# Optimization experiments

Hardware: AMD Instinct MI355X
Metric: run time of the kernel (lower is better)

Reference implementation:

```python
import jax, jax.numpy as jnp
import numpy as np

FILTERS = 256
B, H, W = 16, 64, 64
LN_EPS = 1e-5


def setup_inputs() -> dict:
    key = jax.random.key(0)
    ks = jax.random.split(key, 6)
    C = FILTERS
    scale = 1.0 / np.sqrt(C)  # kaiming-ish init for 1x1 convs
    return {
        "x": jax.random.normal(ks[0], (B, C, H, W), dtype=jnp.float32),
        "g": jax.random.normal(ks[1], (B, C, H, W), dtype=jnp.float32),
        "Wx": jax.random.normal(ks[2], (C, C), dtype=jnp.float32) * scale,
        "Wg": jax.random.normal(ks[3], (C, C), dtype=jnp.float32) * scale,
        "Wpsi": jax.random.normal(ks[4], (1, C), dtype=jnp.float32) * scale,
        "ln_gamma": jnp.ones((C,), dtype=jnp.float32),
        "ln_beta": jnp.zeros((C,), dtype=jnp.float32),
        "bxg": jnp.zeros((C,), dtype=jnp.float32),
        "bpsi": jnp.zeros((1,), dtype=jnp.float32),
    }


def reference(x, g, Wx, Wg, Wpsi, ln_gamma, ln_beta, bxg, bpsi):
    # 1x1 convs == per-pixel channel GEMMs: [B,C,H,W] x [O,C] -> [B,O,H,W]
    x_conv = jnp.einsum("bchw,oc->bohw", x, Wx)
    g_conv = jnp.einsum("bchw,oc->bohw", g, Wg)
    att = jax.nn.relu(x_conv + g_conv + bxg[None, :, None, None])
    # LayerNorm over channel dim (original permutes to NHWC, LN over last dim)
    mean = jnp.mean(att, axis=1, keepdims=True)
    var = jnp.mean(jnp.square(att - mean), axis=1, keepdims=True)
    att = (att - mean) * jax.lax.rsqrt(var + LN_EPS)
    att = att * ln_gamma[None, :, None, None] + ln_beta[None, :, None, None]
    # psi: 1x1 conv to single channel + bias, sigmoid gate
    att = jnp.einsum("bchw,oc->bohw", att, Wpsi) + bpsi[None, :, None, None]
    att = jax.nn.sigmoid(att)  # [B,1,H,W]
    return att * x
```

## Files before the change

kernel.cpp:

```cpp
#include <hip/hip_runtime.h>
#include <stdint.h>


typedef __bf16 bf16x8 __attribute__((ext_vector_type(8)));
typedef float f32x4 __attribute__((ext_vector_type(4)));

#define STR2 264
#define LN_EPS 1e-5f

__device__ __forceinline__ uint16_t f2b(float f) {
    union { float f; uint32_t i; } v; v.f = f;
    uint32_t x = v.i;
    return (uint16_t)((x + 0x7FFFu + ((x >> 16) & 1u)) >> 16);
}

struct EpiShared {
    float red[3][4][64];
    float cpart[8];
};

union ALds {
    uint16_t a[2][64 * STR2];
    EpiShared e;
};

__global__ void wconv_kernel(const float* __restrict__ Wx, const float* __restrict__ Wg,
                             uint16_t* __restrict__ ox, uint16_t* __restrict__ og) {
    const int i  = blockIdx.x * 256 + threadIdx.x;
    const int n  = i >> 6;
    const int k4 = (i & 63) * 4;
    const int it = k4 >> 5;
    const int kk = k4 & 31;
    const int dst = it * 8192 + n * 32 + kk;
    const float4 a = *(const float4*)&Wx[n * 256 + k4];
    const float4 b = *(const float4*)&Wg[n * 256 + k4];
    uint2 pa, pb;
    pa.x = (uint32_t)f2b(a.x) | ((uint32_t)f2b(a.y) << 16);
    pa.y = (uint32_t)f2b(a.z) | ((uint32_t)f2b(a.w) << 16);
    pb.x = (uint32_t)f2b(b.x) | ((uint32_t)f2b(b.y) << 16);
    pb.y = (uint32_t)f2b(b.z) | ((uint32_t)f2b(b.w) << 16);
    *(uint2*)&ox[dst] = pa;
    *(uint2*)&og[dst] = pb;
}

__global__ __launch_bounds__(512, 4) void attgate_psi(
    const float* __restrict__ x,
    const float* __restrict__ g,
    const uint16_t* __restrict__ Wxb,
    const uint16_t* __restrict__ Wgb,
    const float* __restrict__ Wpsi,
    const float* __restrict__ gamma,
    const float* __restrict__ beta,
    const float* __restrict__ bxg,
    const float* __restrict__ bpsi,
    float* __restrict__ psi_g)
{
    __shared__ __align__(16) ALds u;

    const int t    = threadIdx.x;
    const int lane = t & 63;
    const int wv   = t >> 6;
    const int os   = wv & 3;
    const int ps   = wv >> 2;
    const int ln   = lane & 15;
    const int q    = lane >> 4;

    const int gp0  = blockIdx.x * 64;
    const int b    = gp0 >> 12;
    const int pix0 = gp0 & 4095;
    const size_t xbase = (size_t)b * (256 * 4096) + pix0;

    const int at  = t & 255;
    const int px  = at & 63;
    const int cg  = at >> 6;
    const int c0  = cg * 8;
    const float* Asrc = (t < 256) ? x : g;
    const int tens    = (t < 256) ? 0 : 1;

    float av[64];
    #pragma unroll
    for (int it = 0; it < 8; ++it)
        #pragma unroll
        for (int c = 0; c < 8; ++c)
            av[it * 8 + c] = Asrc[xbase + (size_t)(it * 32 + c0 + c) * 4096 + px];

    uint16_t* dstrow = &u.a[tens][px * STR2];
    #pragma unroll
    for (int it = 0; it < 8; ++it) {
        uint4 w;
        w.x = (uint32_t)f2b(av[it*8+0]) | ((uint32_t)f2b(av[it*8+1]) << 16);
        w.y = (uint32_t)f2b(av[it*8+2]) | ((uint32_t)f2b(av[it*8+3]) << 16);
        w.z = (uint32_t)f2b(av[it*8+4]) | ((uint32_t)f2b(av[it*8+5]) << 16);
        w.w = (uint32_t)f2b(av[it*8+6]) | ((uint32_t)f2b(av[it*8+7]) << 16);
        *(uint4*)&dstrow[it * 32 + c0] = w;
    }

    f32x4 acc[2][4];
    #pragma unroll
    for (int i = 0; i < 2; ++i)
        #pragma unroll
        for (int j = 0; j < 4; ++j)
            acc[i][j] = (f32x4){0.f, 0.f, 0.f, 0.f};

    const int fro = os * 64 + ln;

    __syncthreads();

    #pragma unroll
    for (int it = 0; it < 8; ++it) {
        const uint16_t* Wxi = Wxb + it * 8192;
        const uint16_t* Wgi = Wgb + it * 8192;

        bf16x8 bx[4];
        #pragma unroll
        for (int nt = 0; nt < 4; ++nt)
            bx[nt] = *(const bf16x8*)&Wxi[(fro + nt * 16) * 32 + q * 8];

        bf16x8 af[2];
        #pragma unroll
        for (int mt = 0; mt < 2; ++mt)
            af[mt] = *(const bf16x8*)&u.a[0][(ps * 32 + mt * 16 + ln) * STR2 + it * 32 + q * 8];
        #pragma unroll
        for (int mt = 0; mt < 2; ++mt)
            #pragma unroll
            for (int nt = 0; nt < 4; ++nt)
                acc[mt][nt] = __builtin_amdgcn_mfma_f32_16x16x32_bf16(af[mt], bx[nt], acc[mt][nt], 0, 0, 0);

        bf16x8 bg[4];
        #pragma unroll
        for (int nt = 0; nt < 4; ++nt)
            bg[nt] = *(const bf16x8*)&Wgi[(fro + nt * 16) * 32 + q * 8];
        #pragma unroll
        for (int mt = 0; mt < 2; ++mt)
            af[mt] = *(const bf16x8*)&u.a[1][(ps * 32 + mt * 16 + ln) * STR2 + it * 32 + q * 8];
        #pragma unroll
        for (int mt = 0; mt < 2; ++mt)
            #pragma unroll
            for (int nt = 0; nt < 4; ++nt)
                acc[mt][nt] = __builtin_amdgcn_mfma_f32_16x16x32_bf16(af[mt], bg[nt], acc[mt][nt], 0, 0, 0);
    }

    __syncthreads();

    if (t < 256) {
        float a  = Wpsi[t] * gamma[t];
        float bb = Wpsi[t] * beta[t];
        #pragma unroll
        for (int off = 32; off; off >>= 1) {
            a  += __shfl_xor(a, off, 64);
            bb += __shfl_xor(bb, off, 64);
        }
        if (lane == 0) { u.e.cpart[wv] = a; u.e.cpart[4 + wv] = bb; }
    }

    float biasv[4], Ac[4];
    #pragma unroll
    for (int nt = 0; nt < 4; ++nt) {
        const int o = os * 64 + nt * 16 + ln;
        biasv[nt] = bxg[o];
        Ac[nt]    = Wpsi[o] * gamma[o];
    }
    __syncthreads();
    const float sumA = u.e.cpart[0] + u.e.cpart[1] + u.e.cpart[2] + u.e.cpart[3];
    const float sumB = u.e.cpart[4] + u.e.cpart[5] + u.e.cpart[6] + u.e.cpart[7];

    #pragma unroll
    for (int mt = 0; mt < 2; ++mt) {
        #pragma unroll
        for (int r = 0; r < 4; ++r) {
            float s = 0.f, ss = 0.f, tt = 0.f;
            #pragma unroll
            for (int nt = 0; nt < 4; ++nt) {
                float v = acc[mt][nt][r] + biasv[nt];
                v = fmaxf(v, 0.f);
                s += v; ss += v * v; tt += Ac[nt] * v;
            }
            #pragma unroll
            for (int off = 1; off < 16; off <<= 1) {
                s  += __shfl_xor(s,  off, 64);
                ss += __shfl_xor(ss, off, 64);
                tt += __shfl_xor(tt, off, 64);
            }
            if (ln == 0) {
                const int pix = ps * 32 + mt * 16 + q * 4 + r;
                u.e.red[0][os][pix] = s;
                u.e.red[1][os][pix] = ss;
                u.e.red[2][os][pix] = tt;
            }
        }
    }
    __syncthreads();

    if (t < 64) {
        const float s  = u.e.red[0][0][t] + u.e.red[0][1][t] + u.e.red[0][2][t] + u.e.red[0][3][t];
        const float ss = u.e.red[1][0][t] + u.e.red[1][1][t] + u.e.red[1][2][t] + u.e.red[1][3][t];
        const float tt = u.e.red[2][0][t] + u.e.red[2][1][t] + u.e.red[2][2][t] + u.e.red[2][3][t];
        const float mu   = s * (1.f / 256.f);
        const float var  = ss * (1.f / 256.f) - mu * mu;
        const float rstd = rsqrtf(var + LN_EPS);
        const float z    = rstd * (tt - mu * sumA) + sumB + bpsi[0];
        psi_g[gp0 + t] = 1.f / (1.f + __expf(-z));
    }
}

__global__ __launch_bounds__(256) void gate_mul(
    const float* __restrict__ x,
    const float* __restrict__ psi,
    float* __restrict__ out)
{
    const float4* __restrict__ x4  = (const float4*)x;
    float4* __restrict__ o4        = (float4*)out;
    int i = blockIdx.x * 256 + threadIdx.x;
    #pragma unroll 1
    for (; i < 4194304; i += 524288) {
        const int b   = i >> 18;
        const int rem = i & 262143;
        const int p4  = rem & 1023;
        const float4 pv = *(const float4*)&psi[(b << 12) + (p4 << 2)];
        const float4 xv = x4[i];
        float4 o;
        o.x = xv.x * pv.x; o.y = xv.y * pv.y; o.z = xv.z * pv.z; o.w = xv.w * pv.w;
        o4[i] = o;
    }
}

extern "C" void kernel_launch(void* const* d_in, const int* in_sizes, int n_in,
                              void* d_out, int out_size, void* d_ws, size_t ws_size,
                              hipStream_t stream) {
    const float* x    = (const float*)d_in[0];
    const float* g    = (const float*)d_in[1];
    const float* Wx   = (const float*)d_in[2];
    const float* Wg   = (const float*)d_in[3];
    const float* Wpsi = (const float*)d_in[4];
    const float* gam  = (const float*)d_in[5];
    const float* bet  = (const float*)d_in[6];
    const float* bxg  = (const float*)d_in[7];
    const float* bpsi = (const float*)d_in[8];
    float* out        = (float*)d_out;

    uint16_t* Wxb = (uint16_t*)d_ws;
    uint16_t* Wgb = (uint16_t*)((char*)d_ws + 131072);
    float*    psi = (float*)((char*)d_ws + 262144);

    wconv_kernel<<<dim3(64), dim3(256), 0, stream>>>(Wx, Wg, Wxb, Wgb);
    attgate_psi<<<dim3(1024), dim3(512), 0, stream>>>(
        x, g, Wxb, Wgb, Wpsi, gam, bet, bxg, bpsi, psi);
    gate_mul<<<dim3(2048), dim3(256), 0, stream>>>(x, psi, out);
}
```

Measured before the change: 222.9 us.

## Pre-transpose x and g to bf16 pixel-major panels before GEMM kernel

Adds a separate transpose kernel that converts x and g into bf16 and writes them out in pixel-major 64-pixel panels in workspace. The GEMM kernel then fills LDS with contiguous 16-byte loads instead of strided per-channel scalar fp32 loads. The aim is to remove uncoalesced strided global reads from the main kernel. In exchange it adds an extra 64 MB write and read round trip plus one more launch, and it falls back to the old path when the workspace is too small.

```diff
diff --git a/kernel.cpp b/kernel.cpp
--- a/kernel.cpp
+++ b/kernel.cpp
@@ -43,7 +43,190 @@
     *(uint2*)&og[dst] = pb;
 }
 
-__global__ __launch_bounds__(512, 4) void attgate_psi(
+__global__ __launch_bounds__(1024) void transpose_kernel(
+    const float* __restrict__ x, const float* __restrict__ g,
+    uint16_t* __restrict__ ws)
+{
+    const int t    = threadIdx.x;
+    const int lane = t & 63;
+    const int wv   = t >> 6;
+    const int b = blockIdx.x >> 4;
+    const int P = blockIdx.x & 15;
+    const size_t rbase = (size_t)b * (256 * 4096) + (size_t)P * 256 + (size_t)lane * 4;
+    const int pan0 = blockIdx.x * 4;
+
+    #pragma unroll
+    for (int j2 = 0; j2 < 4; ++j2) {
+        const int rg   = wv * 4 + j2;
+        const int tens = rg >> 5;
+        const int cb   = (rg & 31) * 8;
+        const float* __restrict__ src = tens ? g : x;
+
+        float4 v[8];
+        #pragma unroll
+        for (int cc = 0; cc < 8; ++cc)
+            v[cc] = *(const float4*)&src[rbase + (size_t)(cb + cc) * 4096];
+
+        const float* vf = (const float*)v;
+        #pragma unroll
+        for (int j = 0; j < 4; ++j) {
+            uint4 w;
+            w.x = (uint32_t)f2b(vf[0*4+j]) | ((uint32_t)f2b(vf[1*4+j]) << 16);
+            w.y = (uint32_t)f2b(vf[2*4+j]) | ((uint32_t)f2b(vf[3*4+j]) << 16);
+            w.z = (uint32_t)f2b(vf[4*4+j]) | ((uint32_t)f2b(vf[5*4+j]) << 16);
+            w.w = (uint32_t)f2b(vf[6*4+j]) | ((uint32_t)f2b(vf[7*4+j]) << 16);
+            const int px_loc = 4 * lane + j;
+            const int pan    = pan0 + (px_loc >> 6);
+            const int px_in  = px_loc & 63;
+            const size_t off = (((size_t)pan * 2 + tens) * 64 + px_in) * 256 + cb;
+            *(uint4*)&ws[off] = w;
+        }
+    }
+}
+
+__global__ __launch_bounds__(512, 4) void attgate_psi2(
+    const uint16_t* __restrict__ ws,
+    const uint16_t* __restrict__ Wxb,
+    const uint16_t* __restrict__ Wgb,
+    const float* __restrict__ Wpsi,
+    const float* __restrict__ gamma,
+    const float* __restrict__ beta,
+    const float* __restrict__ bxg,
+    const float* __restrict__ bpsi,
+    float* __restrict__ psi_g)
+{
+    __shared__ __align__(16) ALds u;
+
+    const int t    = threadIdx.x;
+    const int lane = t & 63;
+    const int wv   = t >> 6;
+    const int os   = wv & 3;
+    const int ps   = wv >> 2;
+    const int ln   = lane & 15;
+    const int q    = lane >> 4;
+
+    const int gp0 = blockIdx.x * 64;
+
+    const size_t wsbase = (size_t)blockIdx.x * 32768;
+    uint16_t* lds0 = &u.a[0][0];
+    #pragma unroll
+    for (int c = 0; c < 8; ++c) {
+        const int o16 = t + c * 512;
+        const uint4 w = *(const uint4*)&ws[wsbase + (size_t)o16 * 8];
+        const int row = o16 >> 5;
+        const int gch = o16 & 31;
+        *(uint4*)&lds0[row * STR2 + gch * 8] = w;
+    }
+
+    f32x4 acc[2][4];
+    #pragma unroll
+    for (int i = 0; i < 2; ++i)
+        #pragma unroll
+        for (int j = 0; j < 4; ++j)
+            acc[i][j] = (f32x4){0.f, 0.f, 0.f, 0.f};
+
+    const int fro = os * 64 + ln;
+
+    __syncthreads();
+
+    #pragma unroll
+    for (int it = 0; it < 8; ++it) {
+        const uint16_t* Wxi = Wxb + it * 8192;
+        const uint16_t* Wgi = Wgb + it * 8192;
+
+        bf16x8 bx[4];
+        #pragma unroll
+        for (int nt = 0; nt < 4; ++nt)
+            bx[nt] = *(const bf16x8*)&Wxi[(fro + nt * 16) * 32 + q * 8];
+
+        bf16x8 af[2];
+        #pragma unroll
+        for (int mt = 0; mt < 2; ++mt)
+            af[mt] = *(const bf16x8*)&u.a[0][(ps * 32 + mt * 16 + ln) * STR2 + it * 32 + q * 8];
+        #pragma unroll
+        for (int mt = 0; mt < 2; ++mt)
+            #pragma unroll
+            for (int nt = 0; nt < 4; ++nt)
+                acc[mt][nt] = __builtin_amdgcn_mfma_f32_16x16x32_bf16(af[mt], bx[nt], acc[mt][nt], 0, 0, 0);
+
+        bf16x8 bg[4];
+        #pragma unroll
+        for (int nt = 0; nt < 4; ++nt)
+            bg[nt] = *(const bf16x8*)&Wgi[(fro + nt * 16) * 32 + q * 8];
+        #pragma unroll
+        for (int mt = 0; mt < 2; ++mt)
+            af[mt] = *(const bf16x8*)&u.a[1][(ps * 32 + mt * 16 + ln) * STR2 + it * 32 + q * 8];
+        #pragma unroll
+        for (int mt = 0; mt < 2; ++mt)
+            #pragma unroll
+            for (int nt = 0; nt < 4; ++nt)
+                acc[mt][nt] = __builtin_amdgcn_mfma_f32_16x16x32_bf16(af[mt], bg[nt], acc[mt][nt], 0, 0, 0);
+    }
+
+    __syncthreads();
+
+    if (t < 256) {
+        float a  = Wpsi[t] * gamma[t];
+        float bb = Wpsi[t] * beta[t];
+        #pragma unroll
+        for (int off = 32; off; off >>= 1) {
+            a  += __shfl_xor(a, off, 64);
+            bb += __shfl_xor(bb, off, 64);
+        }
+        if (lane == 0) { u.e.cpart[wv] = a; u.e.cpart[4 + wv] = bb; }
+    }
+
+    float biasv[4], Ac[4];
+    #pragma unroll
+    for (int nt = 0; nt < 4; ++nt) {
+        const int o = os * 64 + nt * 16 + ln;
+        biasv[nt] = bxg[o];
+        Ac[nt]    = Wpsi[o] * gamma[o];
+    }
+    __syncthreads();
+    const float sumA = u.e.cpart[0] + u.e.cpart[1] + u.e.cpart[2] + u.e.cpart[3];
+    const float sumB = u.e.cpart[4] + u.e.cpart[5] + u.e.cpart[6] + u.e.cpart[7];
+
+    #pragma unroll
+    for (int mt = 0; mt < 2; ++mt) {
+        #pragma unroll
+        for (int r = 0; r < 4; ++r) {
+            float s = 0.f, ss = 0.f, tt = 0.f;
+            #pragma unroll
+            for (int nt = 0; nt < 4; ++nt) {
+                float v = acc[mt][nt][r] + biasv[nt];
+                v = fmaxf(v, 0.f);
+                s += v; ss += v * v; tt += Ac[nt] * v;
+            }
+            #pragma unroll
+            for (int off = 1; off < 16; off <<= 1) {
+                s  += __shfl_xor(s,  off, 64);
+                ss += __shfl_xor(ss, off, 64);
+                tt += __shfl_xor(tt, off, 64);
+            }
+            if (ln == 0) {
+                const int pix = ps * 32 + mt * 16 + q * 4 + r;
+                u.e.red[0][os][pix] = s;
+                u.e.red[1][os][pix] = ss;
+                u.e.red[2][os][pix] = tt;
+            }
+        }
+    }
+    __syncthreads();
+
+    if (t < 64) {
+        const float s  = u.e.red[0][0][t] + u.e.red[0][1][t] + u.e.red[0][2][t] + u.e.red[0][3][t];
+        const float ss = u.e.red[1][0][t] + u.e.red[1][1][t] + u.e.red[1][2][t] + u.e.red[1][3][t];
+        const float tt = u.e.red[2][0][t] + u.e.red[2][1][t] + u.e.red[2][2][t] + u.e.red[2][3][t];
+        const float mu   = s * (1.f / 256.f);
+        const float var  = ss * (1.f / 256.f) - mu * mu;
+        const float rstd = rsqrtf(var + LN_EPS);
+        const float z    = rstd * (tt - mu * sumA) + sumB + bpsi[0];
+        psi_g[gp0 + t] = 1.f / (1.f + __expf(-z));
+    }
+}
+
+__global__ __launch_bounds__(512, 4) void attgate_psi_fb(
     const float* __restrict__ x,
     const float* __restrict__ g,
     const uint16_t* __restrict__ Wxb,
@@ -103,19 +286,16 @@
             acc[i][j] = (f32x4){0.f, 0.f, 0.f, 0.f};
 
     const int fro = os * 64 + ln;
-
     __syncthreads();
 
     #pragma unroll
     for (int it = 0; it < 8; ++it) {
         const uint16_t* Wxi = Wxb + it * 8192;
         const uint16_t* Wgi = Wgb + it * 8192;
-
         bf16x8 bx[4];
         #pragma unroll
         for (int nt = 0; nt < 4; ++nt)
             bx[nt] = *(const bf16x8*)&Wxi[(fro + nt * 16) * 32 + q * 8];
-
         bf16x8 af[2];
         #pragma unroll
         for (int mt = 0; mt < 2; ++mt)
@@ -125,7 +305,6 @@
             #pragma unroll
             for (int nt = 0; nt < 4; ++nt)
                 acc[mt][nt] = __builtin_amdgcn_mfma_f32_16x16x32_bf16(af[mt], bx[nt], acc[mt][nt], 0, 0, 0);
-
         bf16x8 bg[4];
         #pragma unroll
         for (int nt = 0; nt < 4; ++nt)
@@ -152,7 +331,6 @@
         }
         if (lane == 0) { u.e.cpart[wv] = a; u.e.cpart[4 + wv] = bb; }
     }
-
     float biasv[4], Ac[4];
     #pragma unroll
     for (int nt = 0; nt < 4; ++nt) {
@@ -241,9 +419,18 @@
     uint16_t* Wxb = (uint16_t*)d_ws;
     uint16_t* Wgb = (uint16_t*)((char*)d_ws + 131072);
     float*    psi = (float*)((char*)d_ws + 262144);
+    uint16_t* wsT = (uint16_t*)((char*)d_ws + 524288);
+
+    const size_t need = 524288 + 67108864;
 
     wconv_kernel<<<dim3(64), dim3(256), 0, stream>>>(Wx, Wg, Wxb, Wgb);
-    attgate_psi<<<dim3(1024), dim3(512), 0, stream>>>(
-        x, g, Wxb, Wgb, Wpsi, gam, bet, bxg, bpsi, psi);
+    if (ws_size >= need) {
+        transpose_kernel<<<dim3(256), dim3(1024), 0, stream>>>(x, g, wsT);
+        attgate_psi2<<<dim3(1024), dim3(512), 0, stream>>>(
+            wsT, Wxb, Wgb, Wpsi, gam, bet, bxg, bpsi, psi);
+    } else {
+        attgate_psi_fb<<<dim3(1024), dim3(512), 0, stream>>>(
+            x, g, Wxb, Wgb, Wpsi, gam, bet, bxg, bpsi, psi);
+    }
     gate_mul<<<dim3(2048), dim3(256), 0, stream>>>(x, psi, out);
 }
```

Result: slower. 286.2 us (+28.4%).
